# Kernel tuning notes

Hardware: AMD Instinct MI355X
Metric: run time of the kernel (lower is better)

## Reference

```python
import jax, jax.numpy as jnp
import numpy as np

N = 100000

def gcn_conv(x, src, dst, W, b, n):
    # x: [N, Fin]; src/dst: [E'] (self-loops already included); W: [Fin, Fout]
    h = x @ W  # [N, Fout]
    deg = jax.ops.segment_sum(jnp.ones_like(dst, dtype=h.dtype), dst, num_segments=n)  # [N]
    dinv = deg ** -0.5  # deg >= 1 due to self-loops
    norm = dinv[src] * dinv[dst]  # [E']
    msg = h[src] * norm[:, None]  # gather + scale, [E', Fout]
    out = jax.ops.segment_sum(msg, dst, num_segments=n)  # scatter-add to targets
    return out + b

def setup_inputs() -> dict:
    key = jax.random.key(0)
    k1, k2, k3, k4, k5, k6 = jax.random.split(key, 6)
    x = jax.random.normal(k1, (N, 128), dtype=jnp.float32)
    edge_index = jax.random.randint(k2, (2, 1600000), 0, N, dtype=jnp.int32)
    W1 = jax.random.normal(k3, (128, 64), dtype=jnp.float32) * 0.1
    b1 = jnp.zeros((64,), dtype=jnp.float32)
    W2 = jax.random.normal(k4, (64, 41), dtype=jnp.float32) * 0.1
    b2 = jnp.zeros((41,), dtype=jnp.float32)
    return {"x": x, "edge_index": edge_index, "W1": W1, "b1": b1, "W2": W2, "b2": b2}

def reference(x, edge_index, W1, b1, W2, b2):
    n = x.shape[0]
    loops = jnp.arange(n, dtype=edge_index.dtype)
    src = jnp.concatenate([edge_index[0], loops])  # add self-loops (PyG gcn_norm default)
    dst = jnp.concatenate([edge_index[1], loops])
    # dropout is identity in eval mode (self.training=False)
    h = gcn_conv(x, src, dst, W1, b1, n)
    h = jax.nn.relu(h)
    out = gcn_conv(h, src, dst, W2, b2, n)
    return out
```

## Files before the change

### kernel.cpp

```cpp
#include <hip/hip_runtime.h>


#define FIN 128
#define F1  64
#define F2  41
#define FP  64

#define BSH    8
#define BCAP   6144
#define NBMAX  512
#define CHUNK_P 4096

#define MT 128
#define KC 16

__device__ __forceinline__ unsigned short f2bf(float f) {
    unsigned u = __builtin_bit_cast(unsigned, f);
    u += 0x7FFFu + ((u >> 16) & 1u);
    return (unsigned short)(u >> 16);
}
__device__ __forceinline__ float bf2f(unsigned short h) {
    unsigned u = ((unsigned)h) << 16;
    return __builtin_bit_cast(float, u);
}

__global__ __launch_bounds__(256) void k_partmm1(
    const int* __restrict__ src, const int* __restrict__ dst,
    int* __restrict__ gcur, int* __restrict__ pairs, int E, int nchunks,
    const float* __restrict__ x, const float* __restrict__ W1,
    unsigned short* __restrict__ hs, int n) {
    __shared__ alignas(16) char smem[29760];
    int tid = threadIdx.x;
    if ((int)blockIdx.x < nchunks) {
        int* hist = (int*)smem;
        int* gsh  = hist + NBMAX;
        int* lex  = gsh + NBMAX;
        int* stot = lex + 256;
        int* limg = stot + 4;
        unsigned short* bid = (unsigned short*)(limg + CHUNK_P);
        int e0  = blockIdx.x * CHUNK_P;
        int ds[CHUNK_P / 256], ss[CHUNK_P / 256];
#pragma unroll
        for (int j = 0; j < CHUNK_P / 256; j++) {
            int e = e0 + j * 256 + tid;
            if (e < E) { ds[j] = dst[e]; ss[j] = src[e]; } else ds[j] = -1;
        }
        hist[tid] = 0; hist[tid + 256] = 0;
        __syncthreads();
#pragma unroll
        for (int j = 0; j < CHUNK_P / 256; j++)
            if (ds[j] >= 0) atomicAdd(&hist[ds[j] >> BSH], 1);
        __syncthreads();
        int b0 = 2 * tid, b1 = 2 * tid + 1;
        int c0 = hist[b0], c1 = hist[b1];
        int s  = c0 + c1;
        lex[tid] = s;
        __syncthreads();
        for (int off = 1; off < 256; off <<= 1) {
            int v = lex[tid];
            int a = (tid >= off) ? lex[tid - off] : 0;
            __syncthreads();
            lex[tid] = v + a;
            __syncthreads();
        }
        int incl = lex[tid];
        if (tid == 255) stot[0] = incl;
        int ex = incl - s;
        int l0 = ex, l1 = ex + c0;
        int g0 = c0 ? atomicAdd(&gcur[b0], c0) : 0;
        int g1 = c1 ? atomicAdd(&gcur[b1], c1) : 0;
        hist[b0] = l0; hist[b1] = l1;
        gsh[b0]  = b0 * BCAP + g0 - l0;
        gsh[b1]  = b1 * BCAP + g1 - l1;
        __syncthreads();
#pragma unroll
        for (int j = 0; j < CHUNK_P / 256; j++) {
            if (ds[j] >= 0) {
                int b = ds[j] >> BSH;
                int p = atomicAdd(&hist[b], 1);
                limg[p] = (ss[j] << BSH) | (ds[j] & 255);
                bid[p]  = (unsigned short)b;
            }
        }
        __syncthreads();
        int tot = stot[0];
        for (int k = tid; k < tot; k += 256)
            pairs[k + gsh[bid[k]]] = limg[k];
    } else {
        float* Ws = (float*)smem;
        float (*As)[MT] = (float(*)[MT])(smem + 64 * F1 * 4);
        int n0 = ((int)blockIdx.x - nchunks) * MT;
        int m0 = (tid & 15) * 8;
        int c0 = (tid >> 4) * 4;
        int m_l = tid & 127;
        int kh  = (tid >> 7) * 8;
        bool mvalid = (n0 + m_l) < n;
        float acc[8][4] = {};
        for (int half = 0; half < 2; half++) {
            __syncthreads();
#pragma unroll
            for (int j = 0; j < 4; j++) {
                int f = j * 256 + tid;
                ((float4*)Ws)[f] = ((const float4*)W1)[half * 1024 + f];
            }
            const float* xrow = x + (size_t)(n0 + m_l) * FIN + half * 64 + kh;
            for (int kc = 0; kc < 64; kc += KC) {
                __syncthreads();
                float4 v0 = mvalid ? *(const float4*)(xrow + kc)     : float4{0.f,0.f,0.f,0.f};
                float4 v1 = mvalid ? *(const float4*)(xrow + kc + 4) : float4{0.f,0.f,0.f,0.f};
                As[kh + 0][m_l] = v0.x; As[kh + 1][m_l] = v0.y;
                As[kh + 2][m_l] = v0.z; As[kh + 3][m_l] = v0.w;
                As[kh + 4][m_l] = v1.x; As[kh + 5][m_l] = v1.y;
                As[kh + 6][m_l] = v1.z; As[kh + 7][m_l] = v1.w;
                __syncthreads();
#pragma unroll
                for (int k = 0; k < KC; k++) {
                    float4 a0 = *(const float4*)&As[k][m0];
                    float4 a1 = *(const float4*)&As[k][m0 + 4];
                    float4 w  = *(const float4*)&Ws[(kc + k) * F1 + c0];
                    float a[8] = {a0.x, a0.y, a0.z, a0.w, a1.x, a1.y, a1.z, a1.w};
#pragma unroll
                    for (int i = 0; i < 8; i++) {
                        acc[i][0] += a[i] * w.x;
                        acc[i][1] += a[i] * w.y;
                        acc[i][2] += a[i] * w.z;
                        acc[i][3] += a[i] * w.w;
                    }
                }
            }
        }
#pragma unroll
        for (int i = 0; i < 8; i++) {
            int node = n0 + m0 + i;
            if (node < n) {
                ushort4 o = { f2bf(acc[i][0]), f2bf(acc[i][1]),
                              f2bf(acc[i][2]), f2bf(acc[i][3]) };
                *(ushort4*)&hs[((size_t)node << 6) + c0] = o;
            }
        }
    }
}

__global__ __launch_bounds__(256) void k_build(
    const int* __restrict__ gcur, const int* __restrict__ pairs,
    int* __restrict__ adjcur, int* __restrict__ adj,
    int2* __restrict__ rowinfo, float* __restrict__ dinv, int n) {
    __shared__ int lcnt[256];
    __shared__ int lex[256];
    __shared__ int lcur[256];
    __shared__ int ladj[BCAP];
    __shared__ int sbase;
    int tid = threadIdx.x;
    int b   = blockIdx.x;
    int cntb  = gcur[b]; if (cntb > BCAP) cntb = BCAP;
    int node0 = b << BSH;
    const int* pb = pairs + (size_t)b * BCAP;

    if (tid == 0) sbase = atomicAdd(adjcur, cntb);
    lcnt[tid] = 0;
    __syncthreads();
    for (int k = tid; k < cntb; k += 256) atomicAdd(&lcnt[pb[k] & 255], 1);
    __syncthreads();
    int own = lcnt[tid];
    lex[tid] = own;
    __syncthreads();
    for (int off = 1; off < 256; off <<= 1) {
        int val = lex[tid];
        int add = (tid >= off) ? lex[tid - off] : 0;
        __syncthreads();
        lex[tid] = val + add;
        __syncthreads();
    }
    int excl = lex[tid] - own;
    __syncthreads();
    lex[tid]  = excl;
    lcur[tid] = excl;
    __syncthreads();
    for (int k = tid; k < cntb; k += 256) {
        int pk  = pb[k];
        int pos = atomicAdd(&lcur[pk & 255], 1);
        ladj[pos] = pk >> BSH;
    }
    __syncthreads();
    int base = sbase;
    for (int k = tid; k < cntb; k += 256) adj[base + k] = ladj[k];
    int node = node0 + tid;
    if (node < n) {
        rowinfo[node] = make_int2(base + excl, own);
        dinv[node]    = rsqrtf((float)own + 1.0f);
    }
}

__global__ __launch_bounds__(256) void k_agg1(
    const int2* __restrict__ rowinfo, const int* __restrict__ adj,
    const unsigned short* __restrict__ hs, const float* __restrict__ dinv,
    const float* __restrict__ b1, unsigned short* __restrict__ h1b, int n, int E) {
    int node = blockIdx.x * 4 + (threadIdx.x >> 6);
    if (node >= n) return;
    int lane = threadIdx.x & 63;
    int grp  = lane >> 4;
    int p4   = (lane & 15) * 4;
    int2 ri = rowinfo[node];
    int beg = ri.x, deg = ri.y;
    float dvn = dinv[node];
    float4 acc = {0.f, 0.f, 0.f, 0.f};
    if (grp == 0) {
        ushort4 u = *(const ushort4*)&hs[((size_t)node << 6) + p4];
        acc.x = dvn * bf2f(u.x); acc.y = dvn * bf2f(u.y);
        acc.z = dvn * bf2f(u.z); acc.w = dvn * bf2f(u.w);
    }
    for (int base = 0; base < deg; base += 64) {
        int m = deg - base; if (m > 64) m = 64;
        int idx = beg + base + lane;
        int sidx  = adj[idx < E ? idx : 0];
        float mydv = dinv[sidx];
        int myoff  = sidx << 6;
        int e = 0;
        for (; e + 16 <= m; e += 16) {
            int o0 = __shfl(myoff, e + grp),      o1 = __shfl(myoff, e + 4 + grp);
            int o2 = __shfl(myoff, e + 8 + grp),  o3 = __shfl(myoff, e + 12 + grp);
            float d0 = __shfl(mydv, e + grp),     d1 = __shfl(mydv, e + 4 + grp);
            float d2 = __shfl(mydv, e + 8 + grp), d3 = __shfl(mydv, e + 12 + grp);
            ushort4 u0 = *(const ushort4*)&hs[(size_t)o0 + p4];
            ushort4 u1 = *(const ushort4*)&hs[(size_t)o1 + p4];
            ushort4 u2 = *(const ushort4*)&hs[(size_t)o2 + p4];
            ushort4 u3 = *(const ushort4*)&hs[(size_t)o3 + p4];
            acc.x += d0*bf2f(u0.x) + d1*bf2f(u1.x) + d2*bf2f(u2.x) + d3*bf2f(u3.x);
            acc.y += d0*bf2f(u0.y) + d1*bf2f(u1.y) + d2*bf2f(u2.y) + d3*bf2f(u3.y);
            acc.z += d0*bf2f(u0.z) + d1*bf2f(u1.z) + d2*bf2f(u2.z) + d3*bf2f(u3.z);
            acc.w += d0*bf2f(u0.w) + d1*bf2f(u1.w) + d2*bf2f(u2.w) + d3*bf2f(u3.w);
        }
        for (; e < m; e += 4) {
            int sl = e + grp;
            int o = __shfl(myoff, sl);
            float d = __shfl(mydv, sl);
            if (sl < m) {
                ushort4 u = *(const ushort4*)&hs[(size_t)o + p4];
                acc.x += d * bf2f(u.x); acc.y += d * bf2f(u.y);
                acc.z += d * bf2f(u.z); acc.w += d * bf2f(u.w);
            }
        }
    }
    acc.x += __shfl_xor(acc.x, 16); acc.y += __shfl_xor(acc.y, 16);
    acc.z += __shfl_xor(acc.z, 16); acc.w += __shfl_xor(acc.w, 16);
    acc.x += __shfl_xor(acc.x, 32); acc.y += __shfl_xor(acc.y, 32);
    acc.z += __shfl_xor(acc.z, 32); acc.w += __shfl_xor(acc.w, 32);
    if (grp == 0) {
        float4 bg = *(const float4*)&b1[p4];
        float vx = acc.x * dvn + bg.x; vx = vx > 0.f ? vx : 0.f;
        float vy = acc.y * dvn + bg.y; vy = vy > 0.f ? vy : 0.f;
        float vz = acc.z * dvn + bg.z; vz = vz > 0.f ? vz : 0.f;
        float vw = acc.w * dvn + bg.w; vw = vw > 0.f ? vw : 0.f;
        ushort4 o = { f2bf(vx), f2bf(vy), f2bf(vz), f2bf(vw) };
        *(ushort4*)&h1b[((size_t)node << 6) + p4] = o;
    }
}

__global__ __launch_bounds__(256) void k_mm2(
    const unsigned short* __restrict__ h1b, const float* __restrict__ W2,
    const float* __restrict__ dinv, unsigned short* __restrict__ hs2, int n) {
    __shared__ float Ws[F1 * FP];
    __shared__ float As[KC][MT];
    int t  = threadIdx.x;
    int n0 = blockIdx.x * MT;
    for (int idx = t; idx < F1 * FP; idx += 256) {
        int k = idx >> 6, c = idx & 63;
        Ws[idx] = (c < F2) ? W2[k * F2 + c] : 0.f;
    }
    int m0 = (t & 15) * 8;
    int c0 = (t >> 4) * 4;
    int m_l = t & 127;
    int kh  = (t >> 7) * 8;
    bool mvalid = (n0 + m_l) < n;
    const unsigned short* hrow = h1b + ((size_t)(n0 + m_l) << 6) + kh;
    float acc[8][4] = {};
    for (int kc = 0; kc < F1; kc += KC) {
        __syncthreads();
        ushort4 u0 = mvalid ? *(const ushort4*)(hrow + kc)     : ushort4{0,0,0,0};
        ushort4 u1 = mvalid ? *(const ushort4*)(hrow + kc + 4) : ushort4{0,0,0,0};
        As[kh + 0][m_l] = bf2f(u0.x); As[kh + 1][m_l] = bf2f(u0.y);
        As[kh + 2][m_l] = bf2f(u0.z); As[kh + 3][m_l] = bf2f(u0.w);
        As[kh + 4][m_l] = bf2f(u1.x); As[kh + 5][m_l] = bf2f(u1.y);
        As[kh + 6][m_l] = bf2f(u1.z); As[kh + 7][m_l] = bf2f(u1.w);
        __syncthreads();
#pragma unroll
        for (int k = 0; k < KC; k++) {
            float4 a0 = *(const float4*)&As[k][m0];
            float4 a1 = *(const float4*)&As[k][m0 + 4];
            float4 w  = *(const float4*)&Ws[(kc + k) * FP + c0];
            float a[8] = {a0.x, a0.y, a0.z, a0.w, a1.x, a1.y, a1.z, a1.w};
#pragma unroll
            for (int i = 0; i < 8; i++) {
                acc[i][0] += a[i] * w.x;
                acc[i][1] += a[i] * w.y;
                acc[i][2] += a[i] * w.z;
                acc[i][3] += a[i] * w.w;
            }
        }
    }
#pragma unroll
    for (int i = 0; i < 8; i++) {
        int node = n0 + m0 + i;
        if (node < n) {
            float dv = dinv[node];
            ushort4 o = { f2bf(acc[i][0] * dv), f2bf(acc[i][1] * dv),
                          f2bf(acc[i][2] * dv), f2bf(acc[i][3] * dv) };
            *(ushort4*)&hs2[((size_t)node << 6) + c0] = o;
        }
    }
}

__global__ __launch_bounds__(256) void k_agg2(
    const int2* __restrict__ rowinfo, const int* __restrict__ adj,
    const unsigned short* __restrict__ hs2, const float* __restrict__ dinv,
    const float* __restrict__ b2, float* __restrict__ out, int n, int E) {
    int node = blockIdx.x * 4 + (threadIdx.x >> 6);
    if (node >= n) return;
    int lane = threadIdx.x & 63;
    int grp  = lane >> 4;
    int p4   = (lane & 15) * 4;
    int2 ri = rowinfo[node];
    int beg = ri.x, deg = ri.y;
    float4 acc = {0.f, 0.f, 0.f, 0.f};
    if (grp == 0) {
        ushort4 u = *(const ushort4*)&hs2[((size_t)node << 6) + p4];
        acc.x = bf2f(u.x); acc.y = bf2f(u.y); acc.z = bf2f(u.z); acc.w = bf2f(u.w);
    }
    for (int base = 0; base < deg; base += 64) {
        int m = deg - base; if (m > 64) m = 64;
        int idx = beg + base + lane;
        int myoff = adj[idx < E ? idx : 0] << 6;
        int e = 0;
        for (; e + 16 <= m; e += 16) {
            int o0 = __shfl(myoff, e + grp),      o1 = __shfl(myoff, e + 4 + grp);
            int o2 = __shfl(myoff, e + 8 + grp),  o3 = __shfl(myoff, e + 12 + grp);
            ushort4 u0 = *(const ushort4*)&hs2[(size_t)o0 + p4];
            ushort4 u1 = *(const ushort4*)&hs2[(size_t)o1 + p4];
            ushort4 u2 = *(const ushort4*)&hs2[(size_t)o2 + p4];
            ushort4 u3 = *(const ushort4*)&hs2[(size_t)o3 + p4];
            acc.x += (bf2f(u0.x) + bf2f(u1.x)) + (bf2f(u2.x) + bf2f(u3.x));
            acc.y += (bf2f(u0.y) + bf2f(u1.y)) + (bf2f(u2.y) + bf2f(u3.y));
            acc.z += (bf2f(u0.z) + bf2f(u1.z)) + (bf2f(u2.z) + bf2f(u3.z));
            acc.w += (bf2f(u0.w) + bf2f(u1.w)) + (bf2f(u2.w) + bf2f(u3.w));
        }
        for (; e < m; e += 4) {
            int sl = e + grp;
            int o = __shfl(myoff, sl);
            if (sl < m) {
                ushort4 u = *(const ushort4*)&hs2[(size_t)o + p4];
                acc.x += bf2f(u.x); acc.y += bf2f(u.y);
                acc.z += bf2f(u.z); acc.w += bf2f(u.w);
            }
        }
    }
    acc.x += __shfl_xor(acc.x, 16); acc.y += __shfl_xor(acc.y, 16);
    acc.z += __shfl_xor(acc.z, 16); acc.w += __shfl_xor(acc.w, 16);
    acc.x += __shfl_xor(acc.x, 32); acc.y += __shfl_xor(acc.y, 32);
    acc.z += __shfl_xor(acc.z, 32); acc.w += __shfl_xor(acc.w, 32);
    if (grp == 0) {
        float dv = dinv[node];
        float vv[4] = {acc.x, acc.y, acc.z, acc.w};
#pragma unroll
        for (int j = 0; j < 4; j++) {
            int f = p4 + j;
            if (f < F2) out[(size_t)node * F2 + f] = vv[j] * dv + b2[f];
        }
    }
}

extern "C" void kernel_launch(void* const* d_in, const int* in_sizes, int n_in,
                              void* d_out, int out_size, void* d_ws, size_t ws_size,
                              hipStream_t stream) {
    const float* x  = (const float*)d_in[0];
    const int*   ei = (const int*)d_in[1];
    const float* W1 = (const float*)d_in[2];
    const float* b1 = (const float*)d_in[3];
    const float* W2 = (const float*)d_in[4];
    const float* b2 = (const float*)d_in[5];
    float* out = (float*)d_out;

    const int n = in_sizes[0] / FIN;
    const int E = in_sizes[1] / 2;
    const int* src = ei;
    const int* dst = ei + E;
    const int nbuck   = (n + 255) >> BSH;
    const int nchunks = (E + CHUNK_P - 1) / CHUNK_P;
    const int nmm     = (n + MT - 1) / MT;
    const int nagg    = (n + 3) / 4;

    char* ws = (char*)d_ws;
    size_t off = 0;
    auto alloc = [&](size_t bytes) {
        void* p = ws + off;
        off = (off + bytes + 511) & ~(size_t)511;
        return p;
    };
    int*   gcur    = (int*)alloc((size_t)(NBMAX + 1) * 4);
    int*   pairs   = (int*)alloc((size_t)nbuck * BCAP * 4);
    int*   adj     = (int*)alloc((size_t)E * 4);
    int2*  rowinfo = (int2*)alloc((size_t)n * 8);
    float* dinv    = (float*)alloc((size_t)n * 4);
    unsigned short* hs1 = (unsigned short*)alloc((size_t)n * FP * 2);
    unsigned short* hs2 = (unsigned short*)alloc((size_t)n * FP * 2);
    unsigned short* h1b = (unsigned short*)alloc((size_t)n * FP * 2);

    hipMemsetAsync(gcur, 0, (size_t)(NBMAX + 1) * 4, stream);
    k_partmm1<<<nchunks + nmm, 256, 0, stream>>>(src, dst, gcur, pairs, E, nchunks,
                                                 x, W1, hs1, n);
    k_build<<<nbuck, 256, 0, stream>>>(gcur, pairs, gcur + NBMAX, adj, rowinfo, dinv, n);
    k_agg1<<<nagg, 256, 0, stream>>>(rowinfo, adj, hs1, dinv, b1, h1b, n, E);
    k_mm2<<<nmm, 256, 0, stream>>>(h1b, W2, dinv, hs2, n);
    k_agg2<<<nagg, 256, 0, stream>>>(rowinfo, adj, hs2, dinv, b2, out, n, E);
}
```

Before: 293.1 us.

## Fuse all GCN stages into one persistent cooperative kernel with grid syncs

Replaces the memset and five separate kernel launches with a single cooperative persistent kernel. Blocks loop over work units and use grid-wide syncs between the partition+GEMM1, CSR build, scaling, aggregation-1, GEMM2 and aggregation-2 stages. A new stage pre-scales hs1 by dinv in place, and the first aggregation then applies dinv only at the end. The goal is to remove launch gaps and tail effects between kernels. The cost is six grid barriers, an extra read and write pass over hs1, and lower occupancy and parallelism, since the grid is capped by occupancy times 256 CUs.

```diff
diff --git a/kernel.cpp b/kernel.cpp
--- a/kernel.cpp
+++ b/kernel.cpp
@@ -1,4 +1,7 @@
 #include <hip/hip_runtime.h>
+#include <hip/hip_cooperative_groups.h>
+
+namespace cg = cooperative_groups;
 
 
 #define FIN 128
@@ -13,6 +16,8 @@
 
 #define MT 128
 #define KC 16
+
+#define SMEM_BYTES 29952
 
 __device__ __forceinline__ unsigned short f2bf(float f) {
     unsigned u = __builtin_bit_cast(unsigned, f);
@@ -24,108 +29,302 @@
     return __builtin_bit_cast(float, u);
 }
 
-__global__ __launch_bounds__(256) void k_partmm1(
+__global__ __launch_bounds__(256) void k_all(
     const int* __restrict__ src, const int* __restrict__ dst,
-    int* __restrict__ gcur, int* __restrict__ pairs, int E, int nchunks,
     const float* __restrict__ x, const float* __restrict__ W1,
-    unsigned short* __restrict__ hs, int n) {
-    __shared__ alignas(16) char smem[29760];
-    int tid = threadIdx.x;
-    if ((int)blockIdx.x < nchunks) {
-        int* hist = (int*)smem;
-        int* gsh  = hist + NBMAX;
-        int* lex  = gsh + NBMAX;
-        int* stot = lex + 256;
-        int* limg = stot + 4;
-        unsigned short* bid = (unsigned short*)(limg + CHUNK_P);
-        int e0  = blockIdx.x * CHUNK_P;
-        int ds[CHUNK_P / 256], ss[CHUNK_P / 256];
-#pragma unroll
-        for (int j = 0; j < CHUNK_P / 256; j++) {
-            int e = e0 + j * 256 + tid;
-            if (e < E) { ds[j] = dst[e]; ss[j] = src[e]; } else ds[j] = -1;
-        }
-        hist[tid] = 0; hist[tid + 256] = 0;
-        __syncthreads();
-#pragma unroll
-        for (int j = 0; j < CHUNK_P / 256; j++)
-            if (ds[j] >= 0) atomicAdd(&hist[ds[j] >> BSH], 1);
-        __syncthreads();
-        int b0 = 2 * tid, b1 = 2 * tid + 1;
-        int c0 = hist[b0], c1 = hist[b1];
-        int s  = c0 + c1;
-        lex[tid] = s;
+    const float* __restrict__ b1, const float* __restrict__ W2,
+    const float* __restrict__ b2, float* __restrict__ out,
+    int* __restrict__ gcur, int* __restrict__ pairs, int* __restrict__ adj,
+    int2* __restrict__ rowinfo, float* __restrict__ dinv,
+    unsigned short* __restrict__ hs1, unsigned short* __restrict__ hs2,
+    unsigned short* __restrict__ h1b,
+    int n, int E, int nchunks, int nmm, int nbuck, int nagg) {
+    cg::grid_group gg = cg::this_grid();
+    __shared__ alignas(16) char smem[SMEM_BYTES];
+    const int tid = threadIdx.x;
+    const int NB  = gridDim.x;
+
+    {
+        int i = blockIdx.x * 256 + tid;
+        if (i <= NBMAX) gcur[i] = 0;
+    }
+    gg.sync();
+
+    for (int unit = blockIdx.x; unit < nchunks + nmm; unit += NB) {
+        __syncthreads();
+        if (unit < nchunks) {
+            int* hist = (int*)smem;
+            int* gsh  = hist + NBMAX;
+            int* lex  = gsh + NBMAX;
+            int* stot = lex + 256;
+            int* limg = stot + 4;
+            unsigned short* bid = (unsigned short*)(limg + CHUNK_P);
+            int e0 = unit * CHUNK_P;
+            int ds[CHUNK_P / 256], ss[CHUNK_P / 256];
+#pragma unroll
+            for (int j = 0; j < CHUNK_P / 256; j++) {
+                int e = e0 + j * 256 + tid;
+                if (e < E) { ds[j] = dst[e]; ss[j] = src[e]; } else ds[j] = -1;
+            }
+            hist[tid] = 0; hist[tid + 256] = 0;
+            __syncthreads();
+#pragma unroll
+            for (int j = 0; j < CHUNK_P / 256; j++)
+                if (ds[j] >= 0) atomicAdd(&hist[ds[j] >> BSH], 1);
+            __syncthreads();
+            int b0 = 2 * tid, b1i = 2 * tid + 1;
+            int c0 = hist[b0], c1 = hist[b1i];
+            int s  = c0 + c1;
+            lex[tid] = s;
+            __syncthreads();
+            for (int off = 1; off < 256; off <<= 1) {
+                int v = lex[tid];
+                int a = (tid >= off) ? lex[tid - off] : 0;
+                __syncthreads();
+                lex[tid] = v + a;
+                __syncthreads();
+            }
+            int incl = lex[tid];
+            if (tid == 255) stot[0] = incl;
+            int ex = incl - s;
+            int g0 = c0 ? atomicAdd(&gcur[b0], c0) : 0;
+            int g1 = c1 ? atomicAdd(&gcur[b1i], c1) : 0;
+            hist[b0]  = ex; hist[b1i] = ex + c0;
+            gsh[b0]   = b0 * BCAP + g0 - ex;
+            gsh[b1i]  = b1i * BCAP + g1 - (ex + c0);
+            __syncthreads();
+#pragma unroll
+            for (int j = 0; j < CHUNK_P / 256; j++) {
+                if (ds[j] >= 0) {
+                    int b = ds[j] >> BSH;
+                    int p = atomicAdd(&hist[b], 1);
+                    limg[p] = (ss[j] << BSH) | (ds[j] & 255);
+                    bid[p]  = (unsigned short)b;
+                }
+            }
+            __syncthreads();
+            int tot = stot[0];
+            for (int k = tid; k < tot; k += 256)
+                pairs[k + gsh[bid[k]]] = limg[k];
+        } else {
+            float* Ws = (float*)smem;
+            float (*As)[MT] = (float(*)[MT])(smem + 64 * F1 * 4);
+            int n0 = (unit - nchunks) * MT;
+            int m0 = (tid & 15) * 8;
+            int c0 = (tid >> 4) * 4;
+            int m_l = tid & 127;
+            int kh  = (tid >> 7) * 8;
+            bool mvalid = (n0 + m_l) < n;
+            float acc[8][4] = {};
+            for (int half = 0; half < 2; half++) {
+                __syncthreads();
+#pragma unroll
+                for (int j = 0; j < 4; j++) {
+                    int f = j * 256 + tid;
+                    ((float4*)Ws)[f] = ((const float4*)W1)[half * 1024 + f];
+                }
+                const float* xrow = x + (size_t)(n0 + m_l) * FIN + half * 64 + kh;
+                for (int kc = 0; kc < 64; kc += KC) {
+                    __syncthreads();
+                    float4 v0 = mvalid ? *(const float4*)(xrow + kc)     : float4{0.f,0.f,0.f,0.f};
+                    float4 v1 = mvalid ? *(const float4*)(xrow + kc + 4) : float4{0.f,0.f,0.f,0.f};
+                    As[kh + 0][m_l] = v0.x; As[kh + 1][m_l] = v0.y;
+                    As[kh + 2][m_l] = v0.z; As[kh + 3][m_l] = v0.w;
+                    As[kh + 4][m_l] = v1.x; As[kh + 5][m_l] = v1.y;
+                    As[kh + 6][m_l] = v1.z; As[kh + 7][m_l] = v1.w;
+                    __syncthreads();
+#pragma unroll
+                    for (int k = 0; k < KC; k++) {
+                        float4 a0 = *(const float4*)&As[k][m0];
+                        float4 a1 = *(const float4*)&As[k][m0 + 4];
+                        float4 w  = *(const float4*)&Ws[(kc + k) * F1 + c0];
+                        float a[8] = {a0.x, a0.y, a0.z, a0.w, a1.x, a1.y, a1.z, a1.w};
+#pragma unroll
+                        for (int i = 0; i < 8; i++) {
+                            acc[i][0] += a[i] * w.x;
+                            acc[i][1] += a[i] * w.y;
+                            acc[i][2] += a[i] * w.z;
+                            acc[i][3] += a[i] * w.w;
+                        }
+                    }
+                }
+            }
+#pragma unroll
+            for (int i = 0; i < 8; i++) {
+                int node = n0 + m0 + i;
+                if (node < n) {
+                    ushort4 o = { f2bf(acc[i][0]), f2bf(acc[i][1]),
+                                  f2bf(acc[i][2]), f2bf(acc[i][3]) };
+                    *(ushort4*)&hs1[((size_t)node << 6) + c0] = o;
+                }
+            }
+        }
+    }
+    __threadfence();
+    gg.sync();
+
+    for (int b = blockIdx.x; b < nbuck; b += NB) {
+        __syncthreads();
+        int* lcnt = (int*)smem;
+        int* lex  = lcnt + 256;
+        int* lcur = lex + 256;
+        int* ladj = lcur + 256;
+        int* sbase = ladj + BCAP;
+        int cntb = gcur[b]; if (cntb > BCAP) cntb = BCAP;
+        int node0 = b << BSH;
+        const int* pb = pairs + (size_t)b * BCAP;
+        if (tid == 0) sbase[0] = atomicAdd(&gcur[NBMAX], cntb);
+        lcnt[tid] = 0;
+        __syncthreads();
+        for (int k = tid; k < cntb; k += 256) atomicAdd(&lcnt[pb[k] & 255], 1);
+        __syncthreads();
+        int own = lcnt[tid];
+        lex[tid] = own;
         __syncthreads();
         for (int off = 1; off < 256; off <<= 1) {
-            int v = lex[tid];
-            int a = (tid >= off) ? lex[tid - off] : 0;
-            __syncthreads();
-            lex[tid] = v + a;
-            __syncthreads();
-        }
-        int incl = lex[tid];
-        if (tid == 255) stot[0] = incl;
-        int ex = incl - s;
-        int l0 = ex, l1 = ex + c0;
-        int g0 = c0 ? atomicAdd(&gcur[b0], c0) : 0;
-        int g1 = c1 ? atomicAdd(&gcur[b1], c1) : 0;
-        hist[b0] = l0; hist[b1] = l1;
-        gsh[b0]  = b0 * BCAP + g0 - l0;
-        gsh[b1]  = b1 * BCAP + g1 - l1;
-        __syncthreads();
-#pragma unroll
-        for (int j = 0; j < CHUNK_P / 256; j++) {
-            if (ds[j] >= 0) {
-                int b = ds[j] >> BSH;
-                int p = atomicAdd(&hist[b], 1);
-                limg[p] = (ss[j] << BSH) | (ds[j] & 255);
-                bid[p]  = (unsigned short)b;
-            }
-        }
-        __syncthreads();
-        int tot = stot[0];
-        for (int k = tid; k < tot; k += 256)
-            pairs[k + gsh[bid[k]]] = limg[k];
-    } else {
+            int val = lex[tid];
+            int add = (tid >= off) ? lex[tid - off] : 0;
+            __syncthreads();
+            lex[tid] = val + add;
+            __syncthreads();
+        }
+        int excl = lex[tid] - own;
+        __syncthreads();
+        lcur[tid] = excl;
+        __syncthreads();
+        for (int k = tid; k < cntb; k += 256) {
+            int pk  = pb[k];
+            int pos = atomicAdd(&lcur[pk & 255], 1);
+            ladj[pos] = pk >> BSH;
+        }
+        __syncthreads();
+        int base = sbase[0];
+        for (int k = tid; k < cntb; k += 256) adj[base + k] = ladj[k];
+        int node = node0 + tid;
+        if (node < n) {
+            rowinfo[node] = make_int2(base + excl, own);
+            dinv[node]    = rsqrtf((float)own + 1.0f);
+        }
+    }
+    __threadfence();
+    gg.sync();
+
+    {
+        int total = n * 8;
+        for (int u = blockIdx.x * 256 + tid; u < total; u += NB * 256) {
+            int node = u >> 3;
+            int q = (u & 7) * 8;
+            float dv = dinv[node];
+            ushort4* p0 = (ushort4*)&hs1[((size_t)node << 6) + q];
+            ushort4 a = p0[0], b4 = p0[1];
+            a.x = f2bf(bf2f(a.x) * dv);  a.y = f2bf(bf2f(a.y) * dv);
+            a.z = f2bf(bf2f(a.z) * dv);  a.w = f2bf(bf2f(a.w) * dv);
+            b4.x = f2bf(bf2f(b4.x) * dv); b4.y = f2bf(bf2f(b4.y) * dv);
+            b4.z = f2bf(bf2f(b4.z) * dv); b4.w = f2bf(bf2f(b4.w) * dv);
+            p0[0] = a; p0[1] = b4;
+        }
+    }
+    __threadfence();
+    gg.sync();
+
+    {
+        int lane = tid & 63;
+        int grp  = lane >> 4;
+        int p4   = (lane & 15) * 4;
+        for (int u = blockIdx.x; u < nagg; u += NB) {
+            int node = u * 4 + (tid >> 6);
+            if (node >= n) continue;
+            int2 ri = rowinfo[node];
+            int beg = ri.x, deg = ri.y;
+            float4 acc = {0.f, 0.f, 0.f, 0.f};
+            if (grp == 0) {
+                ushort4 uu = *(const ushort4*)&hs1[((size_t)node << 6) + p4];
+                acc.x = bf2f(uu.x); acc.y = bf2f(uu.y);
+                acc.z = bf2f(uu.z); acc.w = bf2f(uu.w);
+            }
+            for (int base = 0; base < deg; base += 64) {
+                int m = deg - base; if (m > 64) m = 64;
+                int idx = beg + base + lane;
+                int myoff = adj[idx < E ? idx : 0] << 6;
+                int e = 0;
+                for (; e + 16 <= m; e += 16) {
+                    int o0 = __shfl(myoff, e + grp),     o1 = __shfl(myoff, e + 4 + grp);
+                    int o2 = __shfl(myoff, e + 8 + grp), o3 = __shfl(myoff, e + 12 + grp);
+                    ushort4 u0 = *(const ushort4*)&hs1[(size_t)o0 + p4];
+                    ushort4 u1 = *(const ushort4*)&hs1[(size_t)o1 + p4];
+                    ushort4 u2 = *(const ushort4*)&hs1[(size_t)o2 + p4];
+                    ushort4 u3 = *(const ushort4*)&hs1[(size_t)o3 + p4];
+                    acc.x += (bf2f(u0.x) + bf2f(u1.x)) + (bf2f(u2.x) + bf2f(u3.x));
+                    acc.y += (bf2f(u0.y) + bf2f(u1.y)) + (bf2f(u2.y) + bf2f(u3.y));
+                    acc.z += (bf2f(u0.z) + bf2f(u1.z)) + (bf2f(u2.z) + bf2f(u3.z));
+                    acc.w += (bf2f(u0.w) + bf2f(u1.w)) + (bf2f(u2.w) + bf2f(u3.w));
+                }
+                for (; e < m; e += 4) {
+                    int sl = e + grp;
+                    int o = __shfl(myoff, sl);
+                    if (sl < m) {
+                        ushort4 uu = *(const ushort4*)&hs1[(size_t)o + p4];
+                        acc.x += bf2f(uu.x); acc.y += bf2f(uu.y);
+                        acc.z += bf2f(uu.z); acc.w += bf2f(uu.w);
+                    }
+                }
+            }
+            acc.x += __shfl_xor(acc.x, 16); acc.y += __shfl_xor(acc.y, 16);
+            acc.z += __shfl_xor(acc.z, 16); acc.w += __shfl_xor(acc.w, 16);
+            acc.x += __shfl_xor(acc.x, 32); acc.y += __shfl_xor(acc.y, 32);
+            acc.z += __shfl_xor(acc.z, 32); acc.w += __shfl_xor(acc.w, 32);
+            if (grp == 0) {
+                float dvn = dinv[node];
+                float4 bg = *(const float4*)&b1[p4];
+                float vx = acc.x * dvn + bg.x; vx = vx > 0.f ? vx : 0.f;
+                float vy = acc.y * dvn + bg.y; vy = vy > 0.f ? vy : 0.f;
+                float vz = acc.z * dvn + bg.z; vz = vz > 0.f ? vz : 0.f;
+                float vw = acc.w * dvn + bg.w; vw = vw > 0.f ? vw : 0.f;
+                ushort4 o = { f2bf(vx), f2bf(vy), f2bf(vz), f2bf(vw) };
+                *(ushort4*)&h1b[((size_t)node << 6) + p4] = o;
+            }
+        }
+    }
+    __threadfence();
+    gg.sync();
+
+    for (int u = blockIdx.x; u < nmm; u += NB) {
+        __syncthreads();
         float* Ws = (float*)smem;
-        float (*As)[MT] = (float(*)[MT])(smem + 64 * F1 * 4);
-        int n0 = ((int)blockIdx.x - nchunks) * MT;
+        float (*As)[MT] = (float(*)[MT])(smem + F1 * FP * 4);
+        int n0 = u * MT;
+        for (int idx = tid; idx < F1 * FP; idx += 256) {
+            int k = idx >> 6, c = idx & 63;
+            Ws[idx] = (c < F2) ? W2[k * F2 + c] : 0.f;
+        }
         int m0 = (tid & 15) * 8;
         int c0 = (tid >> 4) * 4;
         int m_l = tid & 127;
         int kh  = (tid >> 7) * 8;
         bool mvalid = (n0 + m_l) < n;
+        const unsigned short* hrow = h1b + ((size_t)(n0 + m_l) << 6) + kh;
         float acc[8][4] = {};
-        for (int half = 0; half < 2; half++) {
-            __syncthreads();
-#pragma unroll
-            for (int j = 0; j < 4; j++) {
-                int f = j * 256 + tid;
-                ((float4*)Ws)[f] = ((const float4*)W1)[half * 1024 + f];
-            }
-            const float* xrow = x + (size_t)(n0 + m_l) * FIN + half * 64 + kh;
-            for (int kc = 0; kc < 64; kc += KC) {
-                __syncthreads();
-                float4 v0 = mvalid ? *(const float4*)(xrow + kc)     : float4{0.f,0.f,0.f,0.f};
-                float4 v1 = mvalid ? *(const float4*)(xrow + kc + 4) : float4{0.f,0.f,0.f,0.f};
-                As[kh + 0][m_l] = v0.x; As[kh + 1][m_l] = v0.y;
-                As[kh + 2][m_l] = v0.z; As[kh + 3][m_l] = v0.w;
-                As[kh + 4][m_l] = v1.x; As[kh + 5][m_l] = v1.y;
-                As[kh + 6][m_l] = v1.z; As[kh + 7][m_l] = v1.w;
-                __syncthreads();
-#pragma unroll
-                for (int k = 0; k < KC; k++) {
-                    float4 a0 = *(const float4*)&As[k][m0];
-                    float4 a1 = *(const float4*)&As[k][m0 + 4];
-                    float4 w  = *(const float4*)&Ws[(kc + k) * F1 + c0];
-                    float a[8] = {a0.x, a0.y, a0.z, a0.w, a1.x, a1.y, a1.z, a1.w};
-#pragma unroll
-                    for (int i = 0; i < 8; i++) {
-                        acc[i][0] += a[i] * w.x;
-                        acc[i][1] += a[i] * w.y;
-                        acc[i][2] += a[i] * w.z;
-                        acc[i][3] += a[i] * w.w;
-                    }
+        for (int kc = 0; kc < F1; kc += KC) {
+            __syncthreads();
+            ushort4 u0 = mvalid ? *(const ushort4*)(hrow + kc)     : ushort4{0,0,0,0};
+            ushort4 u1 = mvalid ? *(const ushort4*)(hrow + kc + 4) : ushort4{0,0,0,0};
+            As[kh + 0][m_l] = bf2f(u0.x); As[kh + 1][m_l] = bf2f(u0.y);
+            As[kh + 2][m_l] = bf2f(u0.z); As[kh + 3][m_l] = bf2f(u0.w);
+            As[kh + 4][m_l] = bf2f(u1.x); As[kh + 5][m_l] = bf2f(u1.y);
+            As[kh + 6][m_l] = bf2f(u1.z); As[kh + 7][m_l] = bf2f(u1.w);
+            __syncthreads();
+#pragma unroll
+            for (int k = 0; k < KC; k++) {
+                float4 a0 = *(const float4*)&As[k][m0];
+                float4 a1 = *(const float4*)&As[k][m0 + 4];
+                float4 w  = *(const float4*)&Ws[(kc + k) * FP + c0];
+                float a[8] = {a0.x, a0.y, a0.z, a0.w, a1.x, a1.y, a1.z, a1.w};
+#pragma unroll
+                for (int i = 0; i < 8; i++) {
+                    acc[i][0] += a[i] * w.x;
+                    acc[i][1] += a[i] * w.y;
+                    acc[i][2] += a[i] * w.z;
+                    acc[i][3] += a[i] * w.w;
                 }
             }
         }
@@ -133,237 +332,71 @@
         for (int i = 0; i < 8; i++) {
             int node = n0 + m0 + i;
             if (node < n) {
-                ushort4 o = { f2bf(acc[i][0]), f2bf(acc[i][1]),
-                              f2bf(acc[i][2]), f2bf(acc[i][3]) };
-                *(ushort4*)&hs[((size_t)node << 6) + c0] = o;
-            }
-        }
-    }
-}
-
-__global__ __launch_bounds__(256) void k_build(
-    const int* __restrict__ gcur, const int* __restrict__ pairs,
-    int* __restrict__ adjcur, int* __restrict__ adj,
-    int2* __restrict__ rowinfo, float* __restrict__ dinv, int n) {
-    __shared__ int lcnt[256];
-    __shared__ int lex[256];
-    __shared__ int lcur[256];
-    __shared__ int ladj[BCAP];
-    __shared__ int sbase;
-    int tid = threadIdx.x;
-    int b   = blockIdx.x;
-    int cntb  = gcur[b]; if (cntb > BCAP) cntb = BCAP;
-    int node0 = b << BSH;
-    const int* pb = pairs + (size_t)b * BCAP;
-
-    if (tid == 0) sbase = atomicAdd(adjcur, cntb);
-    lcnt[tid] = 0;
-    __syncthreads();
-    for (int k = tid; k < cntb; k += 256) atomicAdd(&lcnt[pb[k] & 255], 1);
-    __syncthreads();
-    int own = lcnt[tid];
-    lex[tid] = own;
-    __syncthreads();
-    for (int off = 1; off < 256; off <<= 1) {
-        int val = lex[tid];
-        int add = (tid >= off) ? lex[tid - off] : 0;
-        __syncthreads();
-        lex[tid] = val + add;
-        __syncthreads();
-    }
-    int excl = lex[tid] - own;
-    __syncthreads();
-    lex[tid]  = excl;
-    lcur[tid] = excl;
-    __syncthreads();
-    for (int k = tid; k < cntb; k += 256) {
-        int pk  = pb[k];
-        int pos = atomicAdd(&lcur[pk & 255], 1);
-        ladj[pos] = pk >> BSH;
-    }
-    __syncthreads();
-    int base = sbase;
-    for (int k = tid; k < cntb; k += 256) adj[base + k] = ladj[k];
-    int node = node0 + tid;
-    if (node < n) {
-        rowinfo[node] = make_int2(base + excl, own);
-        dinv[node]    = rsqrtf((float)own + 1.0f);
-    }
-}
-
-__global__ __launch_bounds__(256) void k_agg1(
-    const int2* __restrict__ rowinfo, const int* __restrict__ adj,
-    const unsigned short* __restrict__ hs, const float* __restrict__ dinv,
-    const float* __restrict__ b1, unsigned short* __restrict__ h1b, int n, int E) {
-    int node = blockIdx.x * 4 + (threadIdx.x >> 6);
-    if (node >= n) return;
-    int lane = threadIdx.x & 63;
-    int grp  = lane >> 4;
-    int p4   = (lane & 15) * 4;
-    int2 ri = rowinfo[node];
-    int beg = ri.x, deg = ri.y;
-    float dvn = dinv[node];
-    float4 acc = {0.f, 0.f, 0.f, 0.f};
-    if (grp == 0) {
-        ushort4 u = *(const ushort4*)&hs[((size_t)node << 6) + p4];
-        acc.x = dvn * bf2f(u.x); acc.y = dvn * bf2f(u.y);
-        acc.z = dvn * bf2f(u.z); acc.w = dvn * bf2f(u.w);
-    }
-    for (int base = 0; base < deg; base += 64) {
-        int m = deg - base; if (m > 64) m = 64;
-        int idx = beg + base + lane;
-        int sidx  = adj[idx < E ? idx : 0];
-        float mydv = dinv[sidx];
-        int myoff  = sidx << 6;
-        int e = 0;
-        for (; e + 16 <= m; e += 16) {
-            int o0 = __shfl(myoff, e + grp),      o1 = __shfl(myoff, e + 4 + grp);
-            int o2 = __shfl(myoff, e + 8 + grp),  o3 = __shfl(myoff, e + 12 + grp);
-            float d0 = __shfl(mydv, e + grp),     d1 = __shfl(mydv, e + 4 + grp);
-            float d2 = __shfl(mydv, e + 8 + grp), d3 = __shfl(mydv, e + 12 + grp);
-            ushort4 u0 = *(const ushort4*)&hs[(size_t)o0 + p4];
-            ushort4 u1 = *(const ushort4*)&hs[(size_t)o1 + p4];
-            ushort4 u2 = *(const ushort4*)&hs[(size_t)o2 + p4];
-            ushort4 u3 = *(const ushort4*)&hs[(size_t)o3 + p4];
-            acc.x += d0*bf2f(u0.x) + d1*bf2f(u1.x) + d2*bf2f(u2.x) + d3*bf2f(u3.x);
-            acc.y += d0*bf2f(u0.y) + d1*bf2f(u1.y) + d2*bf2f(u2.y) + d3*bf2f(u3.y);
-            acc.z += d0*bf2f(u0.z) + d1*bf2f(u1.z) + d2*bf2f(u2.z) + d3*bf2f(u3.z);
-            acc.w += d0*bf2f(u0.w) + d1*bf2f(u1.w) + d2*bf2f(u2.w) + d3*bf2f(u3.w);
-        }
-        for (; e < m; e += 4) {
-            int sl = e + grp;
-            int o = __shfl(myoff, sl);
-            float d = __shfl(mydv, sl);
-            if (sl < m) {
-                ushort4 u = *(const ushort4*)&hs[(size_t)o + p4];
-                acc.x += d * bf2f(u.x); acc.y += d * bf2f(u.y);
-                acc.z += d * bf2f(u.z); acc.w += d * bf2f(u.w);
-            }
-        }
-    }
-    acc.x += __shfl_xor(acc.x, 16); acc.y += __shfl_xor(acc.y, 16);
-    acc.z += __shfl_xor(acc.z, 16); acc.w += __shfl_xor(acc.w, 16);
-    acc.x += __shfl_xor(acc.x, 32); acc.y += __shfl_xor(acc.y, 32);
-    acc.z += __shfl_xor(acc.z, 32); acc.w += __shfl_xor(acc.w, 32);
-    if (grp == 0) {
-        float4 bg = *(const float4*)&b1[p4];
-        float vx = acc.x * dvn + bg.x; vx = vx > 0.f ? vx : 0.f;
-        float vy = acc.y * dvn + bg.y; vy = vy > 0.f ? vy : 0.f;
-        float vz = acc.z * dvn + bg.z; vz = vz > 0.f ? vz : 0.f;
-        float vw = acc.w * dvn + bg.w; vw = vw > 0.f ? vw : 0.f;
-        ushort4 o = { f2bf(vx), f2bf(vy), f2bf(vz), f2bf(vw) };
-        *(ushort4*)&h1b[((size_t)node << 6) + p4] = o;
-    }
-}
-
-__global__ __launch_bounds__(256) void k_mm2(
-    const unsigned short* __restrict__ h1b, const float* __restrict__ W2,
-    const float* __restrict__ dinv, unsigned short* __restrict__ hs2, int n) {
-    __shared__ float Ws[F1 * FP];
-    __shared__ float As[KC][MT];
-    int t  = threadIdx.x;
-    int n0 = blockIdx.x * MT;
-    for (int idx = t; idx < F1 * FP; idx += 256) {
-        int k = idx >> 6, c = idx & 63;
-        Ws[idx] = (c < F2) ? W2[k * F2 + c] : 0.f;
-    }
-    int m0 = (t & 15) * 8;
-    int c0 = (t >> 4) * 4;
-    int m_l = t & 127;
-    int kh  = (t >> 7) * 8;
-    bool mvalid = (n0 + m_l) < n;
-    const unsigned short* hrow = h1b + ((size_t)(n0 + m_l) << 6) + kh;
-    float acc[8][4] = {};
-    for (int kc = 0; kc < F1; kc += KC) {
-        __syncthreads();
-        ushort4 u0 = mvalid ? *(const ushort4*)(hrow + kc)     : ushort4{0,0,0,0};
-        ushort4 u1 = mvalid ? *(const ushort4*)(hrow + kc + 4) : ushort4{0,0,0,0};
-        As[kh + 0][m_l] = bf2f(u0.x); As[kh + 1][m_l] = bf2f(u0.y);
-        As[kh + 2][m_l] = bf2f(u0.z); As[kh + 3][m_l] = bf2f(u0.w);
-        As[kh + 4][m_l] = bf2f(u1.x); As[kh + 5][m_l] = bf2f(u1.y);
-        As[kh + 6][m_l] = bf2f(u1.z); As[kh + 7][m_l] = bf2f(u1.w);
-        __syncthreads();
-#pragma unroll
-        for (int k = 0; k < KC; k++) {
-            float4 a0 = *(const float4*)&As[k][m0];
-            float4 a1 = *(const float4*)&As[k][m0 + 4];
-            float4 w  = *(const float4*)&Ws[(kc + k) * FP + c0];
-            float a[8] = {a0.x, a0.y, a0.z, a0.w, a1.x, a1.y, a1.z, a1.w};
-#pragma unroll
-            for (int i = 0; i < 8; i++) {
-                acc[i][0] += a[i] * w.x;
-                acc[i][1] += a[i] * w.y;
-                acc[i][2] += a[i] * w.z;
-                acc[i][3] += a[i] * w.w;
-            }
-        }
-    }
-#pragma unroll
-    for (int i = 0; i < 8; i++) {
-        int node = n0 + m0 + i;
-        if (node < n) {
-            float dv = dinv[node];
-            ushort4 o = { f2bf(acc[i][0] * dv), f2bf(acc[i][1] * dv),
-                          f2bf(acc[i][2] * dv), f2bf(acc[i][3] * dv) };
-            *(ushort4*)&hs2[((size_t)node << 6) + c0] = o;
-        }
-    }
-}
-
-__global__ __launch_bounds__(256) void k_agg2(
-    const int2* __restrict__ rowinfo, const int* __restrict__ adj,
-    const unsigned short* __restrict__ hs2, const float* __restrict__ dinv,
-    const float* __restrict__ b2, float* __restrict__ out, int n, int E) {
-    int node = blockIdx.x * 4 + (threadIdx.x >> 6);
-    if (node >= n) return;
-    int lane = threadIdx.x & 63;
-    int grp  = lane >> 4;
-    int p4   = (lane & 15) * 4;
-    int2 ri = rowinfo[node];
-    int beg = ri.x, deg = ri.y;
-    float4 acc = {0.f, 0.f, 0.f, 0.f};
-    if (grp == 0) {
-        ushort4 u = *(const ushort4*)&hs2[((size_t)node << 6) + p4];
-        acc.x = bf2f(u.x); acc.y = bf2f(u.y); acc.z = bf2f(u.z); acc.w = bf2f(u.w);
-    }
-    for (int base = 0; base < deg; base += 64) {
-        int m = deg - base; if (m > 64) m = 64;
-        int idx = beg + base + lane;
-        int myoff = adj[idx < E ? idx : 0] << 6;
-        int e = 0;
-        for (; e + 16 <= m; e += 16) {
-            int o0 = __shfl(myoff, e + grp),      o1 = __shfl(myoff, e + 4 + grp);
-            int o2 = __shfl(myoff, e + 8 + grp),  o3 = __shfl(myoff, e + 12 + grp);
-            ushort4 u0 = *(const ushort4*)&hs2[(size_t)o0 + p4];
-            ushort4 u1 = *(const ushort4*)&hs2[(size_t)o1 + p4];
-            ushort4 u2 = *(const ushort4*)&hs2[(size_t)o2 + p4];
-            ushort4 u3 = *(const ushort4*)&hs2[(size_t)o3 + p4];
-            acc.x += (bf2f(u0.x) + bf2f(u1.x)) + (bf2f(u2.x) + bf2f(u3.x));
-            acc.y += (bf2f(u0.y) + bf2f(u1.y)) + (bf2f(u2.y) + bf2f(u3.y));
-            acc.z += (bf2f(u0.z) + bf2f(u1.z)) + (bf2f(u2.z) + bf2f(u3.z));
-            acc.w += (bf2f(u0.w) + bf2f(u1.w)) + (bf2f(u2.w) + bf2f(u3.w));
-        }
-        for (; e < m; e += 4) {
-            int sl = e + grp;
-            int o = __shfl(myoff, sl);
-            if (sl < m) {
-                ushort4 u = *(const ushort4*)&hs2[(size_t)o + p4];
-                acc.x += bf2f(u.x); acc.y += bf2f(u.y);
-                acc.z += bf2f(u.z); acc.w += bf2f(u.w);
-            }
-        }
-    }
-    acc.x += __shfl_xor(acc.x, 16); acc.y += __shfl_xor(acc.y, 16);
-    acc.z += __shfl_xor(acc.z, 16); acc.w += __shfl_xor(acc.w, 16);
-    acc.x += __shfl_xor(acc.x, 32); acc.y += __shfl_xor(acc.y, 32);
-    acc.z += __shfl_xor(acc.z, 32); acc.w += __shfl_xor(acc.w, 32);
-    if (grp == 0) {
-        float dv = dinv[node];
-        float vv[4] = {acc.x, acc.y, acc.z, acc.w};
-#pragma unroll
-        for (int j = 0; j < 4; j++) {
-            int f = p4 + j;
-            if (f < F2) out[(size_t)node * F2 + f] = vv[j] * dv + b2[f];
+                float dv = dinv[node];
+                ushort4 o = { f2bf(acc[i][0] * dv), f2bf(acc[i][1] * dv),
+                              f2bf(acc[i][2] * dv), f2bf(acc[i][3] * dv) };
+                *(ushort4*)&hs2[((size_t)node << 6) + c0] = o;
+            }
+        }
+    }
+    __threadfence();
+    gg.sync();
+
+    {
+        int lane = tid & 63;
+        int grp  = lane >> 4;
+        int p4   = (lane & 15) * 4;
+        for (int u = blockIdx.x; u < nagg; u += NB) {
+            int node = u * 4 + (tid >> 6);
+            if (node >= n) continue;
+            int2 ri = rowinfo[node];
+            int beg = ri.x, deg = ri.y;
+            float4 acc = {0.f, 0.f, 0.f, 0.f};
+            if (grp == 0) {
+                ushort4 uu = *(const ushort4*)&hs2[((size_t)node << 6) + p4];
+                acc.x = bf2f(uu.x); acc.y = bf2f(uu.y);
+                acc.z = bf2f(uu.z); acc.w = bf2f(uu.w);
+            }
+            for (int base = 0; base < deg; base += 64) {
+                int m = deg - base; if (m > 64) m = 64;
+                int idx = beg + base + lane;
+                int myoff = adj[idx < E ? idx : 0] << 6;
+                int e = 0;
+                for (; e + 16 <= m; e += 16) {
+                    int o0 = __shfl(myoff, e + grp),     o1 = __shfl(myoff, e + 4 + grp);
+                    int o2 = __shfl(myoff, e + 8 + grp), o3 = __shfl(myoff, e + 12 + grp);
+                    ushort4 u0 = *(const ushort4*)&hs2[(size_t)o0 + p4];
+                    ushort4 u1 = *(const ushort4*)&hs2[(size_t)o1 + p4];
+                    ushort4 u2 = *(const ushort4*)&hs2[(size_t)o2 + p4];
+                    ushort4 u3 = *(const ushort4*)&hs2[(size_t)o3 + p4];
+                    acc.x += (bf2f(u0.x) + bf2f(u1.x)) + (bf2f(u2.x) + bf2f(u3.x));
+                    acc.y += (bf2f(u0.y) + bf2f(u1.y)) + (bf2f(u2.y) + bf2f(u3.y));
+                    acc.z += (bf2f(u0.z) + bf2f(u1.z)) + (bf2f(u2.z) + bf2f(u3.z));
+                    acc.w += (bf2f(u0.w) + bf2f(u1.w)) + (bf2f(u2.w) + bf2f(u3.w));
+                }
+                for (; e < m; e += 4) {
+                    int sl = e + grp;
+                    int o = __shfl(myoff, sl);
+                    if (sl < m) {
+                        ushort4 uu = *(const ushort4*)&hs2[(size_t)o + p4];
+                        acc.x += bf2f(uu.x); acc.y += bf2f(uu.y);
+                        acc.z += bf2f(uu.z); acc.w += bf2f(uu.w);
+                    }
+                }
+            }
+            acc.x += __shfl_xor(acc.x, 16); acc.y += __shfl_xor(acc.y, 16);
+            acc.z += __shfl_xor(acc.z, 16); acc.w += __shfl_xor(acc.w, 16);
+            acc.x += __shfl_xor(acc.x, 32); acc.y += __shfl_xor(acc.y, 32);
+            acc.z += __shfl_xor(acc.z, 32); acc.w += __shfl_xor(acc.w, 32);
+            if (grp == 0) {
+                float dv = dinv[node];
+                float vv[4] = {acc.x, acc.y, acc.z, acc.w};
+#pragma unroll
+                for (int j = 0; j < 4; j++) {
+                    int f = p4 + j;
+                    if (f < F2) out[(size_t)node * F2 + f] = vv[j] * dv + b2[f];
+                }
+            }
         }
     }
 }
@@ -404,11 +437,22 @@
     unsigned short* hs2 = (unsigned short*)alloc((size_t)n * FP * 2);
     unsigned short* h1b = (unsigned short*)alloc((size_t)n * FP * 2);
 
-    hipMemsetAsync(gcur, 0, (size_t)(NBMAX + 1) * 4, stream);
-    k_partmm1<<<nchunks + nmm, 256, 0, stream>>>(src, dst, gcur, pairs, E, nchunks,
-                                                 x, W1, hs1, n);
-    k_build<<<nbuck, 256, 0, stream>>>(gcur, pairs, gcur + NBMAX, adj, rowinfo, dinv, n);
-    k_agg1<<<nagg, 256, 0, stream>>>(rowinfo, adj, hs1, dinv, b1, h1b, n, E);
-    k_mm2<<<nmm, 256, 0, stream>>>(h1b, W2, dinv, hs2, n);
-    k_agg2<<<nagg, 256, 0, stream>>>(rowinfo, adj, hs2, dinv, b2, out, n, E);
+    int maxB = 0;
+    hipOccupancyMaxActiveBlocksPerMultiprocessor(&maxB, (const void*)k_all, 256, 0);
+    if (maxB < 1) maxB = 1;
+    int grid = maxB * 256;
+    if (grid > nagg) grid = nagg;
+    if (grid < 3) grid = 3;
+
+    int n_ = n, E_ = E, nchunks_ = nchunks, nmm_ = nmm, nbuck_ = nbuck, nagg_ = nagg;
+    void* args[] = {
+        (void*)&src, (void*)&dst, (void*)&x, (void*)&W1, (void*)&b1,
+        (void*)&W2, (void*)&b2, (void*)&out,
+        (void*)&gcur, (void*)&pairs, (void*)&adj, (void*)&rowinfo, (void*)&dinv,
+        (void*)&hs1, (void*)&hs2, (void*)&h1b,
+        (void*)&n_, (void*)&E_, (void*)&nchunks_, (void*)&nmm_,
+        (void*)&nbuck_, (void*)&nagg_
+    };
+    hipLaunchCooperativeKernel((const void*)k_all, dim3(grid), dim3(256),
+                               args, 0, stream);
 }
```

Result: slower. 981.8 us (+235.0%).
